# Kernel tuning notes

Measured on AMD Instinct MI355X. Metric: run time of the kernel, lower is better.

Reference implementation:

```python
import jax, jax.numpy as jnp
from jax import lax
import numpy as np

B, T = 128, 28
N = T - 1  # 27 recurrent steps


def conv(x, w, b, stride=1, pad=1):
    y = lax.conv_general_dilated(x, w, (stride, stride), [(pad, pad), (pad, pad)],
                                 dimension_numbers=('NCHW', 'OIHW', 'NCHW'))
    return y + b[None, :, None, None]


def convT(x, w, b, stride, pad, out_pad):
    # torch ConvTranspose2d: weight layout [in, out, k, k]
    k = w.shape[-1]
    wt = jnp.flip(w, (-2, -1)).transpose(1, 0, 2, 3)  # -> [out, in, k, k]
    lo, hi = k - 1 - pad, k - 1 - pad + out_pad
    y = lax.conv_general_dilated(x, wt, (1, 1), [(lo, hi), (lo, hi)],
                                 lhs_dilation=(stride, stride),
                                 dimension_numbers=('NCHW', 'OIHW', 'NCHW'))
    return y + b[None, :, None, None]


def setup_inputs():
    key = jax.random.key(0)
    ki = iter(jax.random.split(key, 48))
    def cw(o, i, k=3):
        return jax.random.normal(next(ki), (o, i, k, k), jnp.float32) / np.sqrt(i * k * k)
    def bias(o):
        return jax.random.normal(next(ki), (o,), jnp.float32) * 0.02
    H, I = 16 * 8 * 8, 48 * 8 * 8
    return {
        'x': jax.random.uniform(next(ki), (B, T, 3, 32, 32), jnp.float32),
        'eps': jax.random.normal(next(ki), (N, B, 64, 8, 8), jnp.float32),
        'psix1_w': cw(16, 3),  'psix1_b': bias(16),
        'psix2_w': cw(16, 16), 'psix2_b': bias(16),
        'psiz_w': cw(16, 64),  'psiz_b': bias(16),
        'enc1_w': cw(32, 32),  'enc1_b': bias(32),
        'enc2_w': cw(64, 32),  'enc2_b': bias(64),
        'encm_w': cw(64, 64),  'encm_b': bias(64),
        'encv_w': cw(64, 64),  'encv_b': bias(64),
        'pri_w': cw(32, 16),   'pri_b': bias(32),
        'prim_w': cw(64, 32),  'prim_b': bias(64),
        'priv_w': cw(64, 32),  'priv_b': bias(64),
        'dec1_w': jax.random.normal(next(ki), (32, 32, 3, 3), jnp.float32) / np.sqrt(32 * 9),
        'dec1_b': bias(32),
        'dec2_w': jax.random.normal(next(ki), (32, 3, 3, 3), jnp.float32) / np.sqrt(32 * 9),
        'dec2_b': bias(3),
        'gru_wi': jax.random.normal(next(ki), (3 * H, I), jnp.float32) / np.sqrt(I),
        'gru_wh': jax.random.normal(next(ki), (3 * H, H), jnp.float32) / np.sqrt(H),
        'gru_bi': bias(3 * H),
        'gru_bh': bias(3 * H),
    }


def _forward(x, eps, psix1_w, psix1_b, psix2_w, psix2_b, psiz_w, psiz_b,
             enc1_w, enc1_b, enc2_w, enc2_b, encm_w, encm_b, encv_w, encv_b,
             pri_w, pri_b, prim_w, prim_b, priv_w, priv_b,
             dec1_w, dec1_b, dec2_w, dec2_b, gru_wi, gru_wh, gru_bi, gru_bh):
    Bn = x.shape[0]
    Hf = 16 * 8 * 8
    n = x.shape[1] - 1

    def step(carry, inputs):
        h0, dec_prev, _, _, _, _ = carry
        frame, ep, idx = inputs
        cur = jnp.where(idx < 6, frame, dec_prev)
        px = jax.nn.relu(conv(cur, psix1_w, psix1_b, 2, 1))   # [B,16,16,16]
        px = jax.nn.relu(conv(px, psix2_w, psix2_b, 2, 1))    # [B,16,8,8]
        e = jnp.concatenate([px, h0], axis=1)                 # [B,32,8,8]
        e = jax.nn.relu(conv(e, enc1_w, enc1_b))
        e = jax.nn.relu(conv(e, enc2_w, enc2_b))              # [B,64,8,8]
        zm = conv(e, encm_w, encm_b)
        zlv = jax.nn.softplus(conv(e, encv_w, encv_b))
        p = jax.nn.relu(conv(h0, pri_w, pri_b))               # [B,32,8,8]
        pm = conv(p, prim_w, prim_b)
        plv = jax.nn.softplus(conv(p, priv_w, priv_b))
        z = zm + zlv * ep                                     # source's literal reparam (uses logvar, not std)
        zpsi = jax.nn.relu(conv(z, psiz_w, psiz_b))           # [B,16,8,8]
        d = jnp.concatenate([h0, zpsi], axis=1)               # [B,32,8,8]
        d = jax.nn.relu(convT(d, dec1_w, dec1_b, 2, 1, 0))    # 8 -> 15
        dec = jax.nn.sigmoid(convT(d, dec2_w, dec2_b, 2, 0, 1))  # 15 -> 32, [B,3,32,32]
        # GRUCell on flattened concat
        gi = jnp.concatenate([px, zpsi, h0], axis=1).reshape(Bn, -1)  # [B, 48*8*8]
        hf = h0.reshape(Bn, Hf)
        gih = gi @ gru_wi.T + gru_bi
        ghh = hf @ gru_wh.T + gru_bh
        ir, iz, inn = jnp.split(gih, 3, axis=1)
        hr, hz, hn = jnp.split(ghh, 3, axis=1)
        r = jax.nn.sigmoid(ir + hr)
        u = jax.nn.sigmoid(iz + hz)
        ng = jnp.tanh(inn + r * hn)
        hnew = ((1.0 - u) * ng + u * hf).reshape(Bn, 16, 8, 8)
        return (hnew, dec, zm, zlv, pm, plv), dec

    h0 = jnp.zeros((Bn, 16, 8, 8), jnp.float32)
    dec0 = jnp.zeros((Bn, 3, 32, 32), jnp.float32)
    s0 = jnp.zeros((Bn, 64, 8, 8), jnp.float32)
    frames = jnp.swapaxes(x[:, :n], 0, 1)  # [N,B,3,32,32]
    (_, _, zm, zlv, pm, plv), decs = lax.scan(
        step, (h0, dec0, s0, s0, s0, s0), (frames, eps, jnp.arange(n)))
    output = jnp.swapaxes(decs, 0, 1)  # [B,N,3,32,32]
    return output, zm, zlv, pm, plv


def reference(x, eps, psix1_w, psix1_b, psix2_w, psix2_b, psiz_w, psiz_b,
              enc1_w, enc1_b, enc2_w, enc2_b, encm_w, encm_b, encv_w, encv_b,
              pri_w, pri_b, prim_w, prim_b, priv_w, priv_b,
              dec1_w, dec1_b, dec2_w, dec2_b, gru_wi, gru_wh, gru_bi, gru_bh):
    return _forward(x, eps, psix1_w, psix1_b, psix2_w, psix2_b, psiz_w, psiz_b,
                    enc1_w, enc1_b, enc2_w, enc2_b, encm_w, encm_b, encv_w, encv_b,
                    pri_w, pri_b, prim_w, prim_b, priv_w, priv_b,
                    dec1_w, dec1_b, dec2_w, dec2_b, gru_wi, gru_wh, gru_bi, gru_bh)
```

## Files before the change

kernel.cpp:

```cpp
#include <hip/hip_runtime.h>

#define NSTEP 27

typedef _Float16 f16;
typedef __attribute__((ext_vector_type(8))) _Float16 f16x8;
typedef __attribute__((ext_vector_type(4))) float f32x4;

#define MFMA(a, b, c) __builtin_amdgcn_mfma_f32_16x16x32_f16(a, b, c, 0, 0, 0)

__device__ __forceinline__ float sigmoidf_(float x) { return 1.0f / (1.0f + expf(-x)); }
__device__ __forceinline__ float softplusf_(float x) { return x > 20.0f ? x : log1pf(expf(x)); }

constexpr long OFF_WI   = 0;
constexpr long OFF_WH   = OFF_WI   + 3072L * 3072;
constexpr long OFF_WPX1 = OFF_WH   + 3072L * 1024;
constexpr long OFF_WPX2 = OFF_WPX1 + 512;
constexpr long OFF_WE1  = OFF_WPX2 + 2560;
constexpr long OFF_WE2  = OFF_WE1  + 9216;
constexpr long OFF_WMV  = OFF_WE2  + 18432;
constexpr long OFF_WPZ  = OFF_WMV  + 73728;
constexpr long OFF_WPRI = OFF_WPZ  + 9216;
constexpr long OFF_WPMV = OFF_WPRI + 5120;
constexpr long OFF_WD1  = OFF_WPMV + 36864;
constexpr long OFF_GI   = OFF_WD1  + 9216;
constexpr long OFF_F16_END = OFF_GI + 128L * 3072;

struct Params {
  const float* frame; long fstride;
  const float* eps_t;
  const f16 *wpx1, *wpx2, *we1, *we2, *wmv, *wpz, *wd1, *wpri, *wpmv, *wiG, *whG;
  const float *bpx1, *bpx2, *be1, *be2, *bm, *bv, *bpz, *bd1;
  const float *d2w, *d2b, *bpri, *bpm, *bpv, *gbi, *gbh;
  float *gih0, *gih1, *ghh;
  float* hG; f16* gi;
  float *out_t, *zm, *zlv, *pm, *plv;
  int t, last;
};

__device__ __forceinline__ void scat8_lds(f16* __restrict__ A, int ldk, int pos, int ic, float val) {
  int py = pos >> 3, px = pos & 7;
  f16 v = (f16)val;
#pragma unroll
  for (int ky = 0; ky < 3; ++ky) {
    int oy = py + 1 - ky;
    if ((unsigned)oy >= 8u) continue;
#pragma unroll
    for (int kx = 0; kx < 3; ++kx) {
      int ox = px + 1 - kx;
      if ((unsigned)ox >= 8u) continue;
      A[(oy * 8 + ox) * ldk + ic * 9 + ky * 3 + kx] = v;
    }
  }
}

__device__ __forceinline__ void scatd1_lds(f16* __restrict__ Ad1, int pos, int ic, float val) {
  const int aof[4] = {0, 2560, 7168, 11776};
  const int Kp[4] = {40, 72, 72, 136};
  int py = pos >> 3, px = pos & 7;
  f16 v = (f16)val;
#pragma unroll
  for (int ky = 0; ky < 3; ++ky) {
    int y = 2 * py + ky - 1;
    if ((unsigned)y >= 15u) continue;
    int cy = y & 1;
    int nky = cy ? 2 : 1;
    int tiy = cy ? (ky >> 1) : 0;
#pragma unroll
    for (int kx = 0; kx < 3; ++kx) {
      int x = 2 * px + kx - 1;
      if ((unsigned)x >= 15u) continue;
      int cx = x & 1;
      int nkx = cx ? 2 : 1;
      int tix = cx ? (kx >> 1) : 0;
      int c = cy * 2 + cx;
      Ad1[aof[c] + ((y >> 1) * 8 + (x >> 1)) * Kp[c] + ic * (nky * nkx) + tiy * nkx + tix] = v;
    }
  }
}

__device__ __forceinline__ void gru_tile(const Params& P, int tau, int lane) {
  int lm = lane & 15, q8 = lane >> 4;
  int z = tau / 192, gw = tau - z * 192;
  int mg = gw & 1, ng = gw >> 1;
  const f16* A = (z == 2) ? P.gi + 2048 : P.gi;
  const f16* B = (z == 2) ? P.whG : P.wiG;
  int K = (z == 2) ? 1024 : 1536;
  int k0 = (z == 1) ? 1536 : 0;
  long ldb = (z == 2) ? 1024 : 3072;
  float* outp = (z == 0) ? P.gih0 : (z == 1) ? P.gih1 : P.ghh;
  int m0 = mg * 64, n0 = ng * 32;
  f32x4 acc[4][2] = {};
  const f16* Ap = A + (long)(m0 + lm) * 3072 + k0 + q8 * 8;
  const f16* Bp = B + (long)(n0 + lm) * ldb + k0 + q8 * 8;
#pragma unroll 2
  for (int k = 0; k < K; k += 32) {
    f16x8 b0 = *(const f16x8*)(Bp + k);
    f16x8 b1 = *(const f16x8*)(Bp + 16 * ldb + k);
#pragma unroll
    for (int i = 0; i < 4; ++i) {
      f16x8 a = *(const f16x8*)(Ap + (long)i * 16 * 3072 + k);
      acc[i][0] = MFMA(a, b0, acc[i][0]);
      acc[i][1] = MFMA(a, b1, acc[i][1]);
    }
  }
#pragma unroll
  for (int i = 0; i < 4; ++i)
#pragma unroll
    for (int j = 0; j < 2; ++j)
#pragma unroll
      for (int r = 0; r < 4; ++r)
        outp[(long)(m0 + i * 16 + q8 * 4 + r) * 3072 + n0 + j * 16 + lm] = acc[i][j][r];
}

__global__ __launch_bounds__(256) void k_wpack(const float* __restrict__ src, f16* __restrict__ dst,
                                               int N, int Ks, int Kd) {
  int tot = N * Kd, stride = gridDim.x * 256;
  for (int i = blockIdx.x * 256 + threadIdx.x; i < tot; i += stride) {
    int n = i / Kd, k = i - n * Kd;
    dst[i] = (k < Ks) ? (f16)src[n * Ks + k] : (f16)0.f;
  }
}

__global__ __launch_bounds__(256) void k_wd1(const float* __restrict__ src, f16* __restrict__ dst) {
  int i = blockIdx.x * 256 + threadIdx.x;
  if (i >= 9216) return;
  int c, base;
  if (i < 1024) { c = 0; base = 0; }
  else if (i < 3072) { c = 1; base = 1024; }
  else if (i < 5120) { c = 2; base = 3072; }
  else { c = 3; base = 5120; }
  const int Kc[4] = {32, 64, 64, 128};
  int j = i - base, K = Kc[c];
  int oc = j / K, k = j - oc * K;
  int cy = c >> 1, cx = c & 1;
  int nky = cy ? 2 : 1, nkx = cx ? 2 : 1, ntap = nky * nkx;
  int ic = k / ntap, tap = k - ic * ntap;
  int tiy = tap / nkx, tix = tap - tiy * nkx;
  int ky = (nky == 1) ? 1 : tiy * 2;
  int kx = (nkx == 1) ? 1 : tix * 2;
  dst[i] = (f16)src[((ic * 32 + oc) * 3 + ky) * 3 + kx];
}

__global__ __launch_bounds__(1024) void k_head(Params P) {
  __shared__ f16 lds[78336];
  f16* hbuf = lds;
  f16* B1 = lds + 1024;
  f16* B2 = lds + 38400;
  f16* B3 = lds + 57344;
  f16* A1 = B3;
  f16* frame = B3 + 10240;
  f16* A2 = B3 + 10240;

  int b = blockIdx.x, tid = threadIdx.x;
  int wv = tid >> 6, lane = tid & 63, lm = lane & 15, q = lane >> 4;
  f32x4 z4 = {};

  {
    int i = tid;
    float hn = 0.f;
    if (P.t) {
      long o = (long)b * 3072 + i;
      float ir  = P.gih0[o] + P.gih1[o] + P.gbi[i];
      float iz  = P.gih0[o + 1024] + P.gih1[o + 1024] + P.gbi[i + 1024];
      float in_ = P.gih0[o + 2048] + P.gih1[o + 2048] + P.gbi[i + 2048];
      float hr  = P.ghh[o] + P.gbh[i];
      float hz  = P.ghh[o + 1024] + P.gbh[i + 1024];
      float hnn = P.ghh[o + 2048] + P.gbh[i + 2048];
      float r = sigmoidf_(ir + hr), u = sigmoidf_(iz + hz);
      float ng = tanhf(in_ + r * hnn);
      hn = (1.f - u) * ng + u * P.hG[b * 1024 + i];
    }
    P.hG[b * 1024 + i] = hn;
    hbuf[i] = (f16)hn;
    P.gi[(long)b * 3072 + 2048 + i] = (f16)hn;
  }
  const float* fr = P.frame + (long)b * P.fstride;
  for (int i = tid; i < 3072; i += 1024) frame[i] = (f16)fr[i];
  __syncthreads();
  if (tid < 512) {
    int row = tid >> 1, half = tid & 1;
    int oy = row >> 4, ox = row & 15;
    f16* rp = A1 + row * 40;
    if (half == 0) {
#pragma unroll
      for (int ic = 0; ic < 2; ++ic)
#pragma unroll
        for (int ky = 0; ky < 3; ++ky) {
          int y = 2 * oy + ky - 1;
#pragma unroll
          for (int kx = 0; kx < 3; ++kx) {
            int x = 2 * ox + kx - 1;
            rp[ic * 9 + ky * 3 + kx] =
                ((unsigned)y < 32u && (unsigned)x < 32u) ? frame[ic * 1024 + y * 32 + x] : (f16)0;
          }
        }
    } else {
#pragma unroll
      for (int ky = 0; ky < 3; ++ky) {
        int y = 2 * oy + ky - 1;
#pragma unroll
        for (int kx = 0; kx < 3; ++kx) {
          int x = 2 * ox + kx - 1;
          rp[18 + ky * 3 + kx] =
              ((unsigned)y < 32u && (unsigned)x < 32u) ? frame[2048 + y * 32 + x] : (f16)0;
        }
      }
#pragma unroll
      for (int k = 27; k < 40; ++k) rp[k] = (f16)0;
    }
  } else {
    int4 zz = {0, 0, 0, 0};
    int t2 = tid - 512;
    for (int i = t2; i < 18944 / 8; i += 512) ((int4*)B2)[i] = zz;
    for (int i = t2; i < 37376 / 8; i += 512) ((int4*)B1)[i] = zz;
  }
  __syncthreads();
  {
    int4 zz = {0, 0, 0, 0};
    for (int i = tid; i < 10752 / 8; i += 1024) ((int4*)A2)[i] = zz;
  }
  __syncthreads();
  scat8_lds(B2, 296, tid & 63, 16 + (tid >> 6), (float)hbuf[tid]);
  {
    f16x8 bf = *(const f16x8*)(P.wpx1 + lm * 32 + q * 8);
    float bb = P.bpx1[lm];
    int mt = wv;
    f16x8 a = *(const f16x8*)(A1 + (mt * 16 + lm) * 40 + q * 8);
    f32x4 acc = MFMA(a, bf, z4);
#pragma unroll
    for (int r = 0; r < 4; ++r) {
      int m = mt * 16 + q * 4 + r;
      float val = fmaxf(acc[r] + bb, 0.f);
      int y = m >> 4, x = m & 15;
      f16 v = (f16)val;
#pragma unroll
      for (int ky = 0; ky < 3; ++ky) {
        int ty = y + 1 - ky;
        if (ty < 0 || (ty & 1)) continue;
        int oy = ty >> 1; if (oy >= 8) continue;
#pragma unroll
        for (int kx = 0; kx < 3; ++kx) {
          int tx = x + 1 - kx;
          if (tx < 0 || (tx & 1)) continue;
          int ox = tx >> 1; if (ox >= 8) continue;
          A2[(oy * 8 + ox) * 168 + lm * 9 + ky * 3 + kx] = v;
        }
      }
    }
  }
  __syncthreads();
  if (wv < 4) {
    f32x4 acc = {};
#pragma unroll
    for (int k = 0; k < 160; k += 32) {
      f16x8 a = *(const f16x8*)(A2 + (wv * 16 + lm) * 168 + k + q * 8);
      f16x8 bf = *(const f16x8*)(P.wpx2 + lm * 160 + k + q * 8);
      acc = MFMA(a, bf, acc);
    }
    float bb = P.bpx2[lm];
#pragma unroll
    for (int r = 0; r < 4; ++r) {
      int pos = wv * 16 + q * 4 + r;
      float val = fmaxf(acc[r] + bb, 0.f);
      P.gi[(long)b * 3072 + lm * 64 + pos] = (f16)val;
      scat8_lds(B2, 296, pos, lm, val);
    }
  }
  __syncthreads();
  {
    int nt = wv & 1, mt = (wv >> 1) & 3;
    f32x4 a0 = {};
    if (wv < 8) {
#pragma unroll
      for (int k = 0; k < 288; k += 32) {
        f16x8 bf = *(const f16x8*)(P.we1 + (nt * 16 + lm) * 288 + k + q * 8);
        f16x8 x0 = *(const f16x8*)(B2 + (mt * 16 + lm) * 296 + k + q * 8);
        a0 = MFMA(x0, bf, a0);
      }
    }
    __syncthreads();
    if (wv < 8) {
      float bb = P.be1[nt * 16 + lm];
#pragma unroll
      for (int r = 0; r < 4; ++r)
        scat8_lds(B2, 296, mt * 16 + q * 4 + r, nt * 16 + lm, fmaxf(a0[r] + bb, 0.f));
    }
  }
  __syncthreads();
  {
    int nt = wv & 3, mh = wv >> 2;
    f32x4 acc = {};
#pragma unroll
    for (int k = 0; k < 288; k += 32) {
      f16x8 bf = *(const f16x8*)(P.we2 + (nt * 16 + lm) * 288 + k + q * 8);
      f16x8 a = *(const f16x8*)(B2 + ((mh)*16 + lm) * 296 + k + q * 8);
      acc = MFMA(a, bf, acc);
    }
    int ch = nt * 16 + lm;
    float bb = P.be2[ch];
#pragma unroll
    for (int r = 0; r < 4; ++r)
      scat8_lds(B1, 584, mh * 16 + q * 4 + r, ch, fmaxf(acc[r] + bb, 0.f));
  }
  __syncthreads();
  {
    f32x4 am = {}, av = {};
    int nq = wv & 3, mh = wv >> 2;
    int ch = nq * 16 + lm;
    const float4 ev = *(const float4*)(P.eps_t + (long)b * 4096 + ch * 64 + mh * 16 + q * 4);
    float evr[4] = {ev.x, ev.y, ev.z, ev.w};
#pragma unroll
    for (int k = 0; k < 576; k += 32) {
      f16x8 bm = *(const f16x8*)(P.wmv + (long)ch * 576 + k + q * 8);
      f16x8 bv = *(const f16x8*)(P.wmv + (long)(64 + ch) * 576 + k + q * 8);
      f16x8 a = *(const f16x8*)(B1 + (mh * 16 + lm) * 584 + k + q * 8);
      am = MFMA(a, bm, am);
      av = MFMA(a, bv, av);
    }
    __syncthreads();
    float bbm = P.bm[ch], bbv = P.bv[ch];
#pragma unroll
    for (int r = 0; r < 4; ++r) {
      int pos = mh * 16 + q * 4 + r;
      float zmv = am[r] + bbm;
      float sp = softplusf_(av[r] + bbv);
      float zval = zmv + sp * evr[r];
      if (P.last) {
        P.zm[(long)b * 4096 + ch * 64 + pos] = zmv;
        P.zlv[(long)b * 4096 + ch * 64 + pos] = sp;
      }
      scat8_lds(B1, 584, pos, ch, zval);
    }
  }
  __syncthreads();
  if (wv < 4) {
    f32x4 acc = {};
#pragma unroll
    for (int k = 0; k < 576; k += 32) {
      f16x8 a = *(const f16x8*)(B1 + (wv * 16 + lm) * 584 + k + q * 8);
      f16x8 bf = *(const f16x8*)(P.wpz + (long)lm * 576 + k + q * 8);
      acc = MFMA(a, bf, acc);
    }
    float bb = P.bpz[lm];
#pragma unroll
    for (int r = 0; r < 4; ++r) {
      int pos = wv * 16 + q * 4 + r;
      float val = fmaxf(acc[r] + bb, 0.f);
      P.gi[(long)b * 3072 + 1024 + lm * 64 + pos] = (f16)val;
    }
  }
}

__global__ __launch_bounds__(1024) void k_tailgru(Params P) {
  __shared__ f16 slds[29696];
  int tid = threadIdx.x;
  int wv = tid >> 6, lane = tid & 63, lm = lane & 15, q = lane >> 4;

  if (blockIdx.x >= 128) {
    if (!P.last) {
      int gb = blockIdx.x - 128;
      int cnt = (gb < 64) ? 5 : 4;
      int base = (gb < 64) ? gb * 5 : 320 + (gb - 64) * 4;
      if (wv < cnt) gru_tile(P, base + wv, lane);
      return;
    }
    int b = blockIdx.x - 128;
    f16* Apri = slds;
    f16* Apmv = slds + 10752;
    const f16* hsrc = P.gi + (long)b * 3072 + 2048;
    if (tid < 64) {
      int py = tid >> 3, px = tid & 7;
      f16* rp = Apri + tid * 168;
      int k = 0;
      for (int ic = 0; ic < 16; ++ic)
        for (int ky = 0; ky < 3; ++ky) {
          int y = py + ky - 1;
          for (int kx = 0; kx < 3; ++kx, ++k) {
            int x = px + kx - 1;
            rp[k] = ((unsigned)y < 8u && (unsigned)x < 8u) ? hsrc[ic * 64 + y * 8 + x] : (f16)0;
          }
        }
      for (; k < 168; ++k) rp[k] = (f16)0;
    }
    {
      int4 zz = {0, 0, 0, 0};
      for (int i = tid; i < 18944 / 8; i += 1024) ((int4*)Apmv)[i] = zz;
    }
    __syncthreads();
    if (wv < 8) {
      int nt = wv & 1, mt = wv >> 1;
      f32x4 a0 = {};
#pragma unroll
      for (int k = 0; k < 160; k += 32) {
        f16x8 bf = *(const f16x8*)(P.wpri + (nt * 16 + lm) * 160 + k + q * 8);
        f16x8 x0 = *(const f16x8*)(Apri + (mt * 16 + lm) * 168 + k + q * 8);
        a0 = MFMA(x0, bf, a0);
      }
      float bb = P.bpri[nt * 16 + lm];
#pragma unroll
      for (int r = 0; r < 4; ++r)
        scat8_lds(Apmv, 296, mt * 16 + q * 4 + r, nt * 16 + lm, fmaxf(a0[r] + bb, 0.f));
    }
    __syncthreads();
    {
      f32x4 am = {}, av = {};
      int nq = wv & 3, mh = wv >> 2;
      int ch = nq * 16 + lm;
#pragma unroll
      for (int k = 0; k < 288; k += 32) {
        f16x8 bm = *(const f16x8*)(P.wpmv + (long)ch * 288 + k + q * 8);
        f16x8 bv = *(const f16x8*)(P.wpmv + (long)(64 + ch) * 288 + k + q * 8);
        f16x8 a = *(const f16x8*)(Apmv + (mh * 16 + lm) * 296 + k + q * 8);
        am = MFMA(a, bm, am);
        av = MFMA(a, bv, av);
      }
      float bbm = P.bpm[ch], bbv = P.bpv[ch];
#pragma unroll
      for (int r = 0; r < 4; ++r) {
        int pos = mh * 16 + q * 4 + r;
        P.pm[(long)b * 4096 + ch * 64 + pos] = am[r] + bbm;
        P.plv[(long)b * 4096 + ch * 64 + pos] = softplusf_(av[r] + bbv);
      }
    }
    return;
  }

  int b = blockIdx.x;
  f16* Ad1 = slds;
  f16* d1f = slds + 20480;
  const f16* gb_ = P.gi + (long)b * 3072;
  {
    int i = tid;
    scatd1_lds(Ad1, i & 63, i >> 6, (float)gb_[2048 + i]);
    scatd1_lds(Ad1, i & 63, 16 + (i >> 6), (float)gb_[1024 + i]);
  }
  __syncthreads();
  {
    int nt = wv & 1, mt = (wv >> 1) & 3, cb = wv >> 3;
#pragma unroll
    for (int cc = 0; cc < 2; ++cc) {
      int c = cb + cc * 2;
      int cy = c >> 1, cx = c & 1;
      int Kc = 32 << (cy + cx);
      int Kp = Kc + 8;
      int aof = cy ? (cx ? 11776 : 7168) : (cx ? 2560 : 0);
      int bof = cy ? (cx ? 5120 : 3072) : (cx ? 1024 : 0);
      f32x4 acc = {};
      for (int k = 0; k < Kc; k += 32) {
        f16x8 a = *(const f16x8*)(Ad1 + aof + (mt * 16 + lm) * Kp + k + q * 8);
        f16x8 bf = *(const f16x8*)(P.wd1 + bof + (nt * 16 + lm) * Kc + k + q * 8);
        acc = MFMA(a, bf, acc);
      }
      int oc = nt * 16 + lm;
      float bb = P.bd1[oc];
#pragma unroll
      for (int r = 0; r < 4; ++r) {
        int m = mt * 16 + q * 4 + r;
        int y = 2 * (m >> 3) + cy, x = 2 * (m & 7) + cx;
        if (y < 15 && x < 15)
          d1f[oc * 240 + y * 15 + x] = (f16)fmaxf(acc[r] + bb, 0.f);
      }
    }
  }
  __syncthreads();
  {
    int p = wv & 3, jh = wv >> 2;
    int cy2 = p >> 1, cx2 = p & 1;
    int lx = lane & 15, ly = lane >> 4;
    int x = 2 * lx + cx2;
    float acc0 = P.d2b[0], acc1 = P.d2b[1], acc2 = P.d2b[2];
    int nky = cy2 ? 1 : 2, nkx = cx2 ? 1 : 2;
    int py = jh * 4 + ly;
    for (int ic = 0; ic < 32; ++ic) {
      const f16* sp = d1f + ic * 240;
      const float* wic = P.d2w + ic * 27;
      for (int ty = 0; ty < nky; ++ty) {
        int ky = cy2 ? 1 : ty * 2;
        int iy = (2 * py + cy2 - ky) >> 1;
        bool yv = (unsigned)iy < 15u;
        for (int tx = 0; tx < nkx; ++tx) {
          int kx = cx2 ? 1 : tx * 2;
          int ix = (x - kx) >> 1;
          if (yv && (unsigned)ix < 15u) {
            float v = (float)sp[iy * 15 + ix];
            acc0 += v * wic[ky * 3 + kx];
            acc1 += v * wic[9 + ky * 3 + kx];
            acc2 += v * wic[18 + ky * 3 + kx];
          }
        }
      }
    }
    int y = 2 * py + cy2;
    P.out_t[(long)b * 82944 + 0 * 1024 + y * 32 + x] = sigmoidf_(acc0);
    P.out_t[(long)b * 82944 + 1 * 1024 + y * 32 + x] = sigmoidf_(acc1);
    P.out_t[(long)b * 82944 + 2 * 1024 + y * 32 + x] = sigmoidf_(acc2);
  }
}

extern "C" void kernel_launch(void* const* d_in, const int* in_sizes, int n_in,
                              void* d_out, int out_size, void* d_ws, size_t ws_size,
                              hipStream_t stream) {
  const float* x       = (const float*)d_in[0];
  const float* eps     = (const float*)d_in[1];
  const float* psix1_w = (const float*)d_in[2];
  const float* psix1_b = (const float*)d_in[3];
  const float* psix2_w = (const float*)d_in[4];
  const float* psix2_b = (const float*)d_in[5];
  const float* psiz_w  = (const float*)d_in[6];
  const float* psiz_b  = (const float*)d_in[7];
  const float* enc1_w  = (const float*)d_in[8];
  const float* enc1_b  = (const float*)d_in[9];
  const float* enc2_w  = (const float*)d_in[10];
  const float* enc2_b  = (const float*)d_in[11];
  const float* encm_w  = (const float*)d_in[12];
  const float* encm_b  = (const float*)d_in[13];
  const float* encv_w  = (const float*)d_in[14];
  const float* encv_b  = (const float*)d_in[15];
  const float* pri_w   = (const float*)d_in[16];
  const float* pri_b   = (const float*)d_in[17];
  const float* prim_w  = (const float*)d_in[18];
  const float* prim_b  = (const float*)d_in[19];
  const float* priv_w  = (const float*)d_in[20];
  const float* priv_b  = (const float*)d_in[21];
  const float* dec1_w  = (const float*)d_in[22];
  const float* dec1_b  = (const float*)d_in[23];
  const float* dec2_w  = (const float*)d_in[24];
  const float* dec2_b  = (const float*)d_in[25];
  const float* gru_wi  = (const float*)d_in[26];
  const float* gru_wh  = (const float*)d_in[27];
  const float* gru_bi  = (const float*)d_in[28];
  const float* gru_bh  = (const float*)d_in[29];

  float* out = (float*)d_out;
  float* zm_out  = out + 10616832;
  float* zlv_out = zm_out + 524288;
  float* pm_out  = zlv_out + 524288;
  float* plv_out = pm_out + 524288;

  f16* ws16 = (f16*)d_ws;
  f16* wi_f  = ws16 + OFF_WI;
  f16* wh_f  = ws16 + OFF_WH;
  f16* w_px1 = ws16 + OFF_WPX1;
  f16* w_px2 = ws16 + OFF_WPX2;
  f16* w_e1  = ws16 + OFF_WE1;
  f16* w_e2  = ws16 + OFF_WE2;
  f16* w_mv  = ws16 + OFF_WMV;
  f16* w_pz  = ws16 + OFF_WPZ;
  f16* w_pri = ws16 + OFF_WPRI;
  f16* w_pmv = ws16 + OFF_WPMV;
  f16* w_d1  = ws16 + OFF_WD1;
  f16* gi    = ws16 + OFF_GI;
  float* fws = (float*)(ws16 + OFF_F16_END);
  float* gih0 = fws;
  float* gih1 = gih0 + 393216;
  float* ghh  = gih1 + 393216;
  float* hG   = ghh + 393216;

  k_wpack<<<2048, 256, 0, stream>>>(gru_wi, wi_f, 3072, 3072, 3072);
  k_wpack<<<1024, 256, 0, stream>>>(gru_wh, wh_f, 3072, 1024, 1024);
  k_wpack<<<2, 256, 0, stream>>>(psix1_w, w_px1, 16, 27, 32);
  k_wpack<<<10, 256, 0, stream>>>(psix2_w, w_px2, 16, 144, 160);
  k_wpack<<<36, 256, 0, stream>>>(enc1_w, w_e1, 32, 288, 288);
  k_wpack<<<72, 256, 0, stream>>>(enc2_w, w_e2, 64, 288, 288);
  k_wpack<<<144, 256, 0, stream>>>(encm_w, w_mv, 64, 576, 576);
  k_wpack<<<144, 256, 0, stream>>>(encv_w, w_mv + 64L * 576, 64, 576, 576);
  k_wpack<<<36, 256, 0, stream>>>(psiz_w, w_pz, 16, 576, 576);
  k_wpack<<<20, 256, 0, stream>>>(pri_w, w_pri, 32, 144, 160);
  k_wpack<<<72, 256, 0, stream>>>(prim_w, w_pmv, 64, 288, 288);
  k_wpack<<<72, 256, 0, stream>>>(priv_w, w_pmv + 64L * 288, 64, 288, 288);
  k_wd1<<<36, 256, 0, stream>>>(dec1_w, w_d1);

  for (int t = 0; t < NSTEP; ++t) {
    Params P;
    P.frame = (t < 6) ? x + (long)t * 3072 : out + (long)(t - 1) * 3072;
    P.fstride = (t < 6) ? 86016 : 82944;
    P.eps_t = eps + (long)t * 524288;
    P.wpx1 = w_px1; P.wpx2 = w_px2; P.we1 = w_e1; P.we2 = w_e2;
    P.wmv = w_mv; P.wpz = w_pz; P.wd1 = w_d1; P.wpri = w_pri; P.wpmv = w_pmv;
    P.wiG = wi_f; P.whG = wh_f;
    P.bpx1 = psix1_b; P.bpx2 = psix2_b; P.be1 = enc1_b; P.be2 = enc2_b;
    P.bm = encm_b; P.bv = encv_b; P.bpz = psiz_b; P.bd1 = dec1_b;
    P.d2w = dec2_w; P.d2b = dec2_b; P.bpri = pri_b; P.bpm = prim_b; P.bpv = priv_b;
    P.gbi = gru_bi; P.gbh = gru_bh;
    P.gih0 = gih0; P.gih1 = gih1; P.ghh = ghh;
    P.hG = hG; P.gi = gi;
    P.out_t = out + (long)t * 3072;
    P.zm = zm_out; P.zlv = zlv_out; P.pm = pm_out; P.plv = plv_out;
    P.t = t; P.last = (t == NSTEP - 1);
    k_head<<<128, 1024, 0, stream>>>(P);
    k_tailgru<<<256, 1024, 0, stream>>>(P);
  }
}
```

Baseline: 2.718 ms.

## Halve tailgru block size to 512 threads and launch more blocks

Shrinks k_tailgru blocks from 1024 to 512 threads and raises the grid from 256 to 416 blocks. GRU tiles move from 4-5 per block to 2 per block across 288 blocks. The decoder and prior paths now give each wave twice the work through extra loop iterations and register accumulators. The aim is better occupancy and load balance on the GRU part, at the cost of more serial work per wave in the per-batch decoder blocks.

Measured after the change: 2.265 ms. 16.7% less time.

```diff
diff --git a/kernel.cpp b/kernel.cpp
--- a/kernel.cpp
+++ b/kernel.cpp
@@ -351,7 +351,7 @@
   }
 }
 
-__global__ __launch_bounds__(1024) void k_tailgru(Params P) {
+__global__ __launch_bounds__(512) void k_tailgru(Params P) {
   __shared__ f16 slds[29696];
   int tid = threadIdx.x;
   int wv = tid >> 6, lane = tid & 63, lm = lane & 15, q = lane >> 4;
@@ -359,11 +359,10 @@
   if (blockIdx.x >= 128) {
     if (!P.last) {
       int gb = blockIdx.x - 128;
-      int cnt = (gb < 64) ? 5 : 4;
-      int base = (gb < 64) ? gb * 5 : 320 + (gb - 64) * 4;
-      if (wv < cnt) gru_tile(P, base + wv, lane);
+      if (wv < 2) gru_tile(P, gb * 2 + wv, lane);
       return;
     }
+    if (blockIdx.x >= 256) return;
     int b = blockIdx.x - 128;
     f16* Apri = slds;
     f16* Apmv = slds + 10752;
@@ -384,10 +383,10 @@
     }
     {
       int4 zz = {0, 0, 0, 0};
-      for (int i = tid; i < 18944 / 8; i += 1024) ((int4*)Apmv)[i] = zz;
+      for (int i = tid; i < 18944 / 8; i += 512) ((int4*)Apmv)[i] = zz;
     }
     __syncthreads();
-    if (wv < 8) {
+    {
       int nt = wv & 1, mt = wv >> 1;
       f32x4 a0 = {};
 #pragma unroll
@@ -403,24 +402,29 @@
     }
     __syncthreads();
     {
-      f32x4 am = {}, av = {};
+      f32x4 am[2] = {}, av[2] = {};
       int nq = wv & 3, mh = wv >> 2;
       int ch = nq * 16 + lm;
 #pragma unroll
       for (int k = 0; k < 288; k += 32) {
         f16x8 bm = *(const f16x8*)(P.wpmv + (long)ch * 288 + k + q * 8);
         f16x8 bv = *(const f16x8*)(P.wpmv + (long)(64 + ch) * 288 + k + q * 8);
-        f16x8 a = *(const f16x8*)(Apmv + (mh * 16 + lm) * 296 + k + q * 8);
-        am = MFMA(a, bm, am);
-        av = MFMA(a, bv, av);
+#pragma unroll
+        for (int mi = 0; mi < 2; ++mi) {
+          f16x8 a = *(const f16x8*)(Apmv + ((mh * 2 + mi) * 16 + lm) * 296 + k + q * 8);
+          am[mi] = MFMA(a, bm, am[mi]);
+          av[mi] = MFMA(a, bv, av[mi]);
+        }
       }
       float bbm = P.bpm[ch], bbv = P.bpv[ch];
 #pragma unroll
-      for (int r = 0; r < 4; ++r) {
-        int pos = mh * 16 + q * 4 + r;
-        P.pm[(long)b * 4096 + ch * 64 + pos] = am[r] + bbm;
-        P.plv[(long)b * 4096 + ch * 64 + pos] = softplusf_(av[r] + bbv);
-      }
+      for (int mi = 0; mi < 2; ++mi)
+#pragma unroll
+        for (int r = 0; r < 4; ++r) {
+          int pos = (mh * 2 + mi) * 16 + q * 4 + r;
+          P.pm[(long)b * 4096 + ch * 64 + pos] = am[mi][r] + bbm;
+          P.plv[(long)b * 4096 + ch * 64 + pos] = softplusf_(av[mi][r] + bbv);
+        }
     }
     return;
   }
@@ -433,22 +437,24 @@
     int i = tid;
     scatd1_lds(Ad1, i & 63, i >> 6, (float)gb_[2048 + i]);
     scatd1_lds(Ad1, i & 63, 16 + (i >> 6), (float)gb_[1024 + i]);
-  }
-  __syncthreads();
-  {
-    int nt = wv & 1, mt = (wv >> 1) & 3, cb = wv >> 3;
-#pragma unroll
-    for (int cc = 0; cc < 2; ++cc) {
-      int c = cb + cc * 2;
+    int i2 = tid + 512;
+    scatd1_lds(Ad1, i2 & 63, i2 >> 6, (float)gb_[2048 + i2]);
+    scatd1_lds(Ad1, i2 & 63, 16 + (i2 >> 6), (float)gb_[1024 + i2]);
+  }
+  __syncthreads();
+  {
+    const int Kc[4] = {32, 64, 64, 128};
+    const int Kp[4] = {40, 72, 72, 136};
+    const int aof[4] = {0, 2560, 7168, 11776};
+    const int bof[4] = {0, 1024, 3072, 5120};
+    int nt = wv & 1, mt = wv >> 1;
+#pragma unroll
+    for (int c = 0; c < 4; ++c) {
       int cy = c >> 1, cx = c & 1;
-      int Kc = 32 << (cy + cx);
-      int Kp = Kc + 8;
-      int aof = cy ? (cx ? 11776 : 7168) : (cx ? 2560 : 0);
-      int bof = cy ? (cx ? 5120 : 3072) : (cx ? 1024 : 0);
       f32x4 acc = {};
-      for (int k = 0; k < Kc; k += 32) {
-        f16x8 a = *(const f16x8*)(Ad1 + aof + (mt * 16 + lm) * Kp + k + q * 8);
-        f16x8 bf = *(const f16x8*)(P.wd1 + bof + (nt * 16 + lm) * Kc + k + q * 8);
+      for (int k = 0; k < Kc[c]; k += 32) {
+        f16x8 a = *(const f16x8*)(Ad1 + aof[c] + (mt * 16 + lm) * Kp[c] + k + q * 8);
+        f16x8 bf = *(const f16x8*)(P.wd1 + bof[c] + (nt * 16 + lm) * Kc[c] + k + q * 8);
         acc = MFMA(a, bf, acc);
       }
       int oc = nt * 16 + lm;
@@ -468,32 +474,42 @@
     int cy2 = p >> 1, cx2 = p & 1;
     int lx = lane & 15, ly = lane >> 4;
     int x = 2 * lx + cx2;
-    float acc0 = P.d2b[0], acc1 = P.d2b[1], acc2 = P.d2b[2];
+    float b0 = P.d2b[0], b1 = P.d2b[1], b2 = P.d2b[2];
+    float acc[2][3];
+#pragma unroll
+    for (int j = 0; j < 2; ++j) { acc[j][0] = b0; acc[j][1] = b1; acc[j][2] = b2; }
     int nky = cy2 ? 1 : 2, nkx = cx2 ? 1 : 2;
-    int py = jh * 4 + ly;
     for (int ic = 0; ic < 32; ++ic) {
       const f16* sp = d1f + ic * 240;
       const float* wic = P.d2w + ic * 27;
       for (int ty = 0; ty < nky; ++ty) {
         int ky = cy2 ? 1 : ty * 2;
-        int iy = (2 * py + cy2 - ky) >> 1;
-        bool yv = (unsigned)iy < 15u;
         for (int tx = 0; tx < nkx; ++tx) {
           int kx = cx2 ? 1 : tx * 2;
           int ix = (x - kx) >> 1;
-          if (yv && (unsigned)ix < 15u) {
-            float v = (float)sp[iy * 15 + ix];
-            acc0 += v * wic[ky * 3 + kx];
-            acc1 += v * wic[9 + ky * 3 + kx];
-            acc2 += v * wic[18 + ky * 3 + kx];
+          bool xv = (unsigned)ix < 15u;
+          float w0 = wic[ky * 3 + kx];
+          float w1 = wic[9 + ky * 3 + kx];
+          float w2 = wic[18 + ky * 3 + kx];
+#pragma unroll
+          for (int j = 0; j < 2; ++j) {
+            int py = (jh * 2 + j) * 4 + ly;
+            int iy = (2 * py + cy2 - ky) >> 1;
+            if (xv && (unsigned)iy < 15u) {
+              float v = (float)sp[iy * 15 + ix];
+              acc[j][0] += v * w0; acc[j][1] += v * w1; acc[j][2] += v * w2;
+            }
           }
         }
       }
     }
-    int y = 2 * py + cy2;
-    P.out_t[(long)b * 82944 + 0 * 1024 + y * 32 + x] = sigmoidf_(acc0);
-    P.out_t[(long)b * 82944 + 1 * 1024 + y * 32 + x] = sigmoidf_(acc1);
-    P.out_t[(long)b * 82944 + 2 * 1024 + y * 32 + x] = sigmoidf_(acc2);
+#pragma unroll
+    for (int j = 0; j < 2; ++j) {
+      int y = 2 * ((jh * 2 + j) * 4 + ly) + cy2;
+#pragma unroll
+      for (int oc = 0; oc < 3; ++oc)
+        P.out_t[(long)b * 82944 + oc * 1024 + y * 32 + x] = sigmoidf_(acc[j][oc]);
+    }
   }
 }
 
@@ -588,6 +604,6 @@
     P.zm = zm_out; P.zlv = zlv_out; P.pm = pm_out; P.plv = plv_out;
     P.t = t; P.last = (t == NSTEP - 1);
     k_head<<<128, 1024, 0, stream>>>(P);
-    k_tailgru<<<256, 1024, 0, stream>>>(P);
-  }
-}
+    k_tailgru<<<416, 512, 0, stream>>>(P);
+  }
+}
```
